# Kernel tuning notes

Hardware: AMD Instinct MI355X
Metric: run time of the kernel (lower is better)

Reference implementation:

```python
import jax, jax.numpy as jnp
import numpy as np

IN_C, DIM, OUT_C, N_PIECES = 3, 256, 256, 20
BATCH, SET_N = 16, 128


def _xavier(k, shape, fan_in, fan_out):
    limit = float(np.sqrt(6.0 / (fan_in + fan_out)))
    return jax.random.uniform(k, shape, jnp.float32, -limit, limit)


def setup_inputs() -> dict:
    key = jax.random.key(0)
    ks = jax.random.split(key, 9)
    return {
        "x": jax.random.normal(ks[0], (BATCH, IN_C, SET_N), jnp.float32),
        "conv1_w": _xavier(ks[1], (DIM, IN_C), IN_C, DIM),
        "conv1_b": jnp.zeros((DIM,), jnp.float32),
        "conv2_w": _xavier(ks[2], (DIM, DIM), DIM, DIM),
        "conv2_b": jnp.zeros((DIM,), jnp.float32),
        "pool_w": jax.random.normal(ks[3], (DIM, N_PIECES + 1), jnp.float32) * 0.1,
        "lin1_w": _xavier(ks[4], (DIM, DIM), DIM, DIM),
        "lin1_b": jnp.zeros((DIM,), jnp.float32),
        "lin2_w": _xavier(ks[5], (OUT_C, DIM), DIM, OUT_C),
        "lin2_b": jnp.zeros((OUT_C,), jnp.float32),
        "cls1_w": _xavier(ks[6], (OUT_C, OUT_C), OUT_C, OUT_C),
        "cls1_b": jnp.zeros((OUT_C,), jnp.float32),
        "cls2_w": _xavier(ks[7], (10, OUT_C), OUT_C, 10),
        "cls2_b": jnp.zeros((10,), jnp.float32),
    }


def _fspool(x, pool_w, tau=1.0):
    # x: (B, C, N); pool_w: (C, N_PIECES+1). n is None -> full sets, mask is all ones.
    B, C, N = x.shape
    # piecewise-linear continuous weights evaluated at ratios i/(N-1)
    ratios = jnp.clip(jnp.arange(N, dtype=x.dtype) / max(N - 1, 1), 0.0, 1.0)  # (N,)
    idx_f = N_PIECES * ratios
    idx = jnp.floor(idx_f).astype(jnp.int32)
    frac = idx_f - idx.astype(x.dtype)
    left = pool_w[:, idx]                                   # (C, N)
    right = pool_w[:, jnp.clip(idx + 1, 0, N_PIECES)]       # (C, N)
    w = (1.0 - frac) * left + frac * right                  # (C, N)
    # relaxed continuous sort (NeuralSort / deterministic_sort), descending
    s = x.reshape(B * C, N, 1)
    A = jnp.abs(s - jnp.swapaxes(s, 1, 2))                  # (BC, N, N)
    Bsum = A.sum(axis=2, keepdims=True)                     # == A @ 1 1^T rowsums, (BC, N, 1)
    scaling = (N + 1 - 2 * (jnp.arange(N) + 1)).astype(x.dtype)  # (N,)
    Cmat = s * scaling[None, None, :]                       # (BC, N, N)
    P = jax.nn.softmax(jnp.swapaxes(Cmat - Bsum, 1, 2) / tau, axis=-1)  # (BC, N, N)
    xs = jnp.matmul(P, s).reshape(B, C, N)                  # soft-sorted, descending
    pooled = (xs * w[None]).sum(axis=2)                     # (B, C)
    return pooled, P


def reference(x, conv1_w, conv1_b, conv2_w, conv2_b, pool_w,
              lin1_w, lin1_b, lin2_w, lin2_b, cls1_w, cls1_b, cls2_w, cls2_b):
    # conv1x1 stack: (B, IN_C, N) -> (B, DIM, N)
    h = jnp.einsum('dc,bcn->bdn', conv1_w, x) + conv1_b[None, :, None]
    h = jax.nn.relu(h)
    h = jnp.einsum('dc,bcn->bdn', conv2_w, h) + conv2_b[None, :, None]
    pooled, _ = _fspool(h, pool_w)                          # (B, DIM)
    z = jax.nn.relu(pooled @ lin1_w.T + lin1_b)
    z = z @ lin2_w.T + lin2_b                               # (B, OUT_C)
    z = jax.nn.relu(z @ cls1_w.T + cls1_b)
    return z @ cls2_w.T + cls2_b                            # (B, 10)
```

## Files before the change

### kernel.cpp

```cpp
#include <hip/hip_runtime.h>
#include <math.h>


#if __has_builtin(__builtin_amdgcn_exp2f)
#define EXP2F(x) __builtin_amdgcn_exp2f(x)
#else
#define EXP2F(x) exp2f(x)
#endif

__device__ __forceinline__ float pool_weight(const float* __restrict__ pw, int j)
{
    float ratio = (float)j / 127.0f;
    float idx_f = 20.0f * ratio;
    int idx = (int)idx_f;
    float frac = idx_f - (float)idx;
    int idx2 = idx + 1 > 20 ? 20 : idx + 1;
    return (1.0f - frac) * pw[idx] + frac * pw[idx2];
}

#define OSTEP(sv, bv, scal, m, se, sd)                      \
    {                                                       \
        float v_  = fmaf((sv), (scal), -(bv));              \
        float mn_ = fmaxf((m), v_);                         \
        float sc_ = EXP2F((m) - mn_);                       \
        float e_  = EXP2F(v_ - mn_);                        \
        (se) = fmaf((se), sc_, e_);                         \
        (sd) = fmaf((sd), sc_, e_ * (sv));                  \
        (m)  = mn_;                                         \
    }

__global__ __launch_bounds__(256) void conv_pool_kernel(
    const float* __restrict__ x,   const float* __restrict__ w1,
    const float* __restrict__ b1,  const float* __restrict__ W2,
    const float* __restrict__ b2,  const float* __restrict__ pool_w,
    float* __restrict__ pooled)
{
    const float LOG2E = 1.4426950408889634f;
    __shared__ float4 w1p[256];
    __shared__ float  Ast[4][32];
    __shared__ float2 Bsp[32][66];
    __shared__ float  ss[4][128];
    __shared__ float  bb[4][128];

    int tid = threadIdx.x;
    int blk = blockIdx.x;
    int b   = blk >> 6;
    int c0  = (blk & 63) << 2;

    int wid = tid >> 6, l = tid & 63;
    int ng  = tid & 31;
    int kg  = tid >> 5;
    int n0  = ng * 2;

    w1p[tid] = make_float4(w1[tid*3], w1[tid*3+1], w1[tid*3+2], b1[tid]);
    const float* xb = x + b * 384;
    float x00 = xb[n0],          x01 = xb[n0 + 1];
    float x0a = xb[n0 + 64],     x0b = xb[n0 + 65];
    float x10 = xb[128 + n0],    x11 = xb[128 + n0 + 1];
    float x1a = xb[128 + n0 + 64], x1b = xb[128 + n0 + 65];
    float x20 = xb[256 + n0],    x21 = xb[256 + n0 + 1];
    float x2a = xb[256 + n0 + 64], x2b = xb[256 + n0 + 65];
    __syncthreads();

    float acc0 = 0.f, acc1 = 0.f;

    for (int k0 = 0; k0 < 256; k0 += 32) {
        if (tid < 128)
            Ast[tid >> 5][tid & 31] =
                W2[(c0 + (tid >> 5)) * 256 + k0 + (tid & 31)];
        #pragma unroll
        for (int q = 0; q < 4; q++) {
            int krel = kg * 4 + q;
            float4 wv = w1p[k0 + krel];
            float h0 = fmaxf(fmaf(wv.x,x00, fmaf(wv.y,x10, fmaf(wv.z,x20, wv.w))), 0.f);
            float h1 = fmaxf(fmaf(wv.x,x01, fmaf(wv.y,x11, fmaf(wv.z,x21, wv.w))), 0.f);
            float ha = fmaxf(fmaf(wv.x,x0a, fmaf(wv.y,x1a, fmaf(wv.z,x2a, wv.w))), 0.f);
            float hb = fmaxf(fmaf(wv.x,x0b, fmaf(wv.y,x1b, fmaf(wv.z,x2b, wv.w))), 0.f);
            *(float4*)&Bsp[krel][n0] = make_float4(h0, ha, h1, hb);
        }
        __syncthreads();
        float4 a4[8];
        #pragma unroll
        for (int q = 0; q < 8; q++)
            a4[q] = *(const float4*)&Ast[wid][q * 4];
        #pragma unroll
        for (int kk = 0; kk < 32; kk++) {
            float a = ((const float*)a4)[kk];
            float2 bv = Bsp[kk][l];
            acc0 = fmaf(a, bv.x, acc0);
            acc1 = fmaf(a, bv.y, acc1);
        }
        __syncthreads();
    }

    float bias = b2[c0 + wid];
    float s0 = acc0 + bias, s1 = acc1 + bias;
    ss[wid][l]      = s0;
    ss[wid][l + 64] = s1;

    float a0=0,a1=0,a2=0,a3=0, g0=0,g1=0,g2=0,g3=0;
    #pragma unroll 8
    for (int j = 0; j < 128; j += 4) {
        float4 s4 = *(const float4*)&ss[wid][j];
        a0 += fabsf(s0 - s4.x); a1 += fabsf(s0 - s4.y);
        a2 += fabsf(s0 - s4.z); a3 += fabsf(s0 - s4.w);
        g0 += fabsf(s1 - s4.x); g1 += fabsf(s1 - s4.y);
        g2 += fabsf(s1 - s4.z); g3 += fabsf(s1 - s4.w);
    }
    bb[wid][l]      = ((a0+a1)+(a2+a3)) * LOG2E;
    bb[wid][l + 64] = ((g0+g1)+(g2+g3)) * LOG2E;

    float scal0 = (float)(127 - 2 * l) * LOG2E;
    float scal1 = (float)(-1 - 2 * l) * LOG2E;
    float mA0=-1e30f, mB0=-1e30f, mA1=-1e30f, mB1=-1e30f;
    float seA0=0,seB0=0,sdA0=0,sdB0=0;
    float seA1=0,seB1=0,sdA1=0,sdB1=0;
    #pragma unroll 4
    for (int i = 0; i < 128; i += 4) {
        float4 s4 = *(const float4*)&ss[wid][i];
        float4 b4 = *(const float4*)&bb[wid][i];
        OSTEP(s4.x, b4.x, scal0, mA0, seA0, sdA0);
        OSTEP(s4.y, b4.y, scal0, mB0, seB0, sdB0);
        OSTEP(s4.z, b4.z, scal0, mA0, seA0, sdA0);
        OSTEP(s4.w, b4.w, scal0, mB0, seB0, sdB0);
        OSTEP(s4.x, b4.x, scal1, mA1, seA1, sdA1);
        OSTEP(s4.y, b4.y, scal1, mB1, seB1, sdB1);
        OSTEP(s4.z, b4.z, scal1, mA1, seA1, sdA1);
        OSTEP(s4.w, b4.w, scal1, mB1, seB1, sdB1);
    }
    float m0  = fmaxf(mA0, mB0);
    float scA = EXP2F(mA0 - m0), scB = EXP2F(mB0 - m0);
    float xs0 = (sdA0 * scA + sdB0 * scB) / (seA0 * scA + seB0 * scB);
    float m1  = fmaxf(mA1, mB1);
    float tA  = EXP2F(mA1 - m1), tB = EXP2F(mB1 - m1);
    float xs1 = (sdA1 * tA + sdB1 * tB) / (seA1 * tA + seB1 * tB);

    int c = c0 + wid;
    const float* pw = pool_w + c * 21;
    float part = xs0 * pool_weight(pw, l) + xs1 * pool_weight(pw, l + 64);
    #pragma unroll
    for (int off = 32; off > 0; off >>= 1)
        part += __shfl_xor(part, off);
    if (l == 0) pooled[b * 256 + c] = part;
}

__device__ __forceinline__ void dense512(
    const float* __restrict__ W, const float* __restrict__ Bv,
    const float* in_lds, float* out_lds, int tid, bool do_relu)
{
    int o = tid >> 1, p = tid & 1;
    const float* wr = W + o * 256 + p * 128;
    const float* ir = in_lds + p * 128;
    float acc = 0.f;
    #pragma unroll
    for (int k = 0; k < 128; k += 4) {
        float4 wv = *(const float4*)(wr + k);
        float4 iv = *(const float4*)(ir + k);
        acc = fmaf(wv.x, iv.x, acc); acc = fmaf(wv.y, iv.y, acc);
        acc = fmaf(wv.z, iv.z, acc); acc = fmaf(wv.w, iv.w, acc);
    }
    acc += __shfl_xor(acc, 1);
    if (p == 0) {
        acc += Bv[o];
        out_lds[o] = do_relu ? fmaxf(acc, 0.f) : acc;
    }
}

__global__ __launch_bounds__(512) void tail_kernel(
    const float* __restrict__ pooled,
    const float* __restrict__ L1w, const float* __restrict__ L1b,
    const float* __restrict__ L2w, const float* __restrict__ L2b,
    const float* __restrict__ C1w, const float* __restrict__ C1b,
    const float* __restrict__ C2w, const float* __restrict__ C2b,
    float* __restrict__ out)
{
    __shared__ float za[256], zb[256];
    int bt = blockIdx.x, tid = threadIdx.x;
    if (tid < 256) za[tid] = pooled[bt * 256 + tid];
    __syncthreads();
    dense512(L1w, L1b, za, zb, tid, true);
    __syncthreads();
    dense512(L2w, L2b, zb, za, tid, false);
    __syncthreads();
    dense512(C1w, C1b, za, zb, tid, true);
    __syncthreads();
    if (tid < 320) {
        int o = tid >> 5, kb = tid & 31;
        const float* wr = C2w + o * 256 + kb * 8;
        const float* ir = zb + kb * 8;
        float4 w0 = *(const float4*)(wr);
        float4 w1v = *(const float4*)(wr + 4);
        float4 i0 = *(const float4*)(ir);
        float4 i1 = *(const float4*)(ir + 4);
        float p = fmaf(w0.x,i0.x, fmaf(w0.y,i0.y, fmaf(w0.z,i0.z,
                  fmaf(w0.w,i0.w, fmaf(w1v.x,i1.x, fmaf(w1v.y,i1.y,
                  fmaf(w1v.z,i1.z, w1v.w*i1.w)))))));
        #pragma unroll
        for (int off = 16; off > 0; off >>= 1)
            p += __shfl_xor(p, off, 32);
        if (kb == 0) out[bt * 10 + o] = p + C2b[o];
    }
}

extern "C" void kernel_launch(void* const* d_in, const int* in_sizes, int n_in,
                              void* d_out, int out_size, void* d_ws, size_t ws_size,
                              hipStream_t stream)
{
    (void)in_sizes; (void)n_in; (void)out_size; (void)ws_size;
    const float* x       = (const float*)d_in[0];
    const float* conv1_w = (const float*)d_in[1];
    const float* conv1_b = (const float*)d_in[2];
    const float* conv2_w = (const float*)d_in[3];
    const float* conv2_b = (const float*)d_in[4];
    const float* pool_w  = (const float*)d_in[5];
    const float* lin1_w  = (const float*)d_in[6];
    const float* lin1_b  = (const float*)d_in[7];
    const float* lin2_w  = (const float*)d_in[8];
    const float* lin2_b  = (const float*)d_in[9];
    const float* cls1_w  = (const float*)d_in[10];
    const float* cls1_b  = (const float*)d_in[11];
    const float* cls2_w  = (const float*)d_in[12];
    const float* cls2_b  = (const float*)d_in[13];
    float* out = (float*)d_out;

    float* pooled = (float*)d_ws;

    conv_pool_kernel<<<1024, 256, 0, stream>>>(
        x, conv1_w, conv1_b, conv2_w, conv2_b, pool_w, pooled);
    tail_kernel<<<16, 512, 0, stream>>>(pooled,
        lin1_w, lin1_b, lin2_w, lin2_b, cls1_w, cls1_b, cls2_w, cls2_b, out);
}
```

Measured before the change: 62.61 us.

## Fuse MLP tail into conv-pool kernel via last-blocks atomic counter gate

Merges the two kernels into one launch. Each block publishes its pooled value and increments a global counter, and the last 16 blocks to arrive each wait for all blocks to finish before running the dense MLP tail for one batch element. This removes the second kernel launch and its gap, but adds a memset launch, a spin-wait, and a serial 256-thread tail running inside the final blocks.

New measurement: 70.12 us. 1.12x slower.

```diff
diff --git a/kernel.cpp b/kernel.cpp
--- a/kernel.cpp
+++ b/kernel.cpp
@@ -7,6 +7,8 @@
 #else
 #define EXP2F(x) exp2f(x)
 #endif
+
+#define NBLK 1024u
 
 __device__ __forceinline__ float pool_weight(const float* __restrict__ pw, int j)
 {
@@ -29,11 +31,16 @@
         (m)  = mn_;                                         \
     }
 
-__global__ __launch_bounds__(256) void conv_pool_kernel(
+__global__ __launch_bounds__(256) void fused_lastgate(
     const float* __restrict__ x,   const float* __restrict__ w1,
     const float* __restrict__ b1,  const float* __restrict__ W2,
     const float* __restrict__ b2,  const float* __restrict__ pool_w,
-    float* __restrict__ pooled)
+    const float* __restrict__ L1w, const float* __restrict__ L1b,
+    const float* __restrict__ L2w, const float* __restrict__ L2b,
+    const float* __restrict__ C1w, const float* __restrict__ C1b,
+    const float* __restrict__ C2w, const float* __restrict__ C2b,
+    float* __restrict__ pooled, unsigned* __restrict__ cnt,
+    float* __restrict__ out)
 {
     const float LOG2E = 1.4426950408889634f;
     __shared__ float4 w1p[256];
@@ -41,6 +48,8 @@
     __shared__ float2 Bsp[32][66];
     __shared__ float  ss[4][128];
     __shared__ float  bb[4][128];
+    __shared__ float  za[256], zb[256];
+    __shared__ unsigned sOld;
 
     int tid = threadIdx.x;
     int blk = blockIdx.x;
@@ -54,11 +63,11 @@
 
     w1p[tid] = make_float4(w1[tid*3], w1[tid*3+1], w1[tid*3+2], b1[tid]);
     const float* xb = x + b * 384;
-    float x00 = xb[n0],          x01 = xb[n0 + 1];
-    float x0a = xb[n0 + 64],     x0b = xb[n0 + 65];
-    float x10 = xb[128 + n0],    x11 = xb[128 + n0 + 1];
+    float x00 = xb[n0],            x01 = xb[n0 + 1];
+    float x0a = xb[n0 + 64],       x0b = xb[n0 + 65];
+    float x10 = xb[128 + n0],      x11 = xb[128 + n0 + 1];
     float x1a = xb[128 + n0 + 64], x1b = xb[128 + n0 + 65];
-    float x20 = xb[256 + n0],    x21 = xb[256 + n0 + 1];
+    float x20 = xb[256 + n0],      x21 = xb[256 + n0 + 1];
     float x2a = xb[256 + n0 + 64], x2b = xb[256 + n0 + 65];
     __syncthreads();
 
@@ -141,64 +150,80 @@
     #pragma unroll
     for (int off = 32; off > 0; off >>= 1)
         part += __shfl_xor(part, off);
-    if (l == 0) pooled[b * 256 + c] = part;
-}
-
-__device__ __forceinline__ void dense512(
-    const float* __restrict__ W, const float* __restrict__ Bv,
-    const float* in_lds, float* out_lds, int tid, bool do_relu)
-{
-    int o = tid >> 1, p = tid & 1;
-    const float* wr = W + o * 256 + p * 128;
-    const float* ir = in_lds + p * 128;
-    float acc = 0.f;
-    #pragma unroll
-    for (int k = 0; k < 128; k += 4) {
-        float4 wv = *(const float4*)(wr + k);
-        float4 iv = *(const float4*)(ir + k);
-        acc = fmaf(wv.x, iv.x, acc); acc = fmaf(wv.y, iv.y, acc);
-        acc = fmaf(wv.z, iv.z, acc); acc = fmaf(wv.w, iv.w, acc);
-    }
-    acc += __shfl_xor(acc, 1);
-    if (p == 0) {
-        acc += Bv[o];
-        out_lds[o] = do_relu ? fmaxf(acc, 0.f) : acc;
-    }
-}
-
-__global__ __launch_bounds__(512) void tail_kernel(
-    const float* __restrict__ pooled,
-    const float* __restrict__ L1w, const float* __restrict__ L1b,
-    const float* __restrict__ L2w, const float* __restrict__ L2b,
-    const float* __restrict__ C1w, const float* __restrict__ C1b,
-    const float* __restrict__ C2w, const float* __restrict__ C2b,
-    float* __restrict__ out)
-{
-    __shared__ float za[256], zb[256];
-    int bt = blockIdx.x, tid = threadIdx.x;
-    if (tid < 256) za[tid] = pooled[bt * 256 + tid];
-    __syncthreads();
-    dense512(L1w, L1b, za, zb, tid, true);
-    __syncthreads();
-    dense512(L2w, L2b, zb, za, tid, false);
-    __syncthreads();
-    dense512(C1w, C1b, za, zb, tid, true);
-    __syncthreads();
-    if (tid < 320) {
-        int o = tid >> 5, kb = tid & 31;
-        const float* wr = C2w + o * 256 + kb * 8;
-        const float* ir = zb + kb * 8;
-        float4 w0 = *(const float4*)(wr);
-        float4 w1v = *(const float4*)(wr + 4);
-        float4 i0 = *(const float4*)(ir);
-        float4 i1 = *(const float4*)(ir + 4);
-        float p = fmaf(w0.x,i0.x, fmaf(w0.y,i0.y, fmaf(w0.z,i0.z,
-                  fmaf(w0.w,i0.w, fmaf(w1v.x,i1.x, fmaf(w1v.y,i1.y,
-                  fmaf(w1v.z,i1.z, w1v.w*i1.w)))))));
-        #pragma unroll
-        for (int off = 16; off > 0; off >>= 1)
-            p += __shfl_xor(p, off, 32);
-        if (kb == 0) out[bt * 10 + o] = p + C2b[o];
+    if (l == 0)
+        __hip_atomic_store(&pooled[b * 256 + c], part,
+                           __ATOMIC_RELAXED, __HIP_MEMORY_SCOPE_AGENT);
+
+    __syncthreads();
+    if (tid == 0)
+        sOld = __hip_atomic_fetch_add(cnt, 1u, __ATOMIC_ACQ_REL,
+                                      __HIP_MEMORY_SCOPE_AGENT);
+    __syncthreads();
+    unsigned old = sOld;
+    if (old < NBLK - 16u) return;
+
+    int bt = (int)(old - (NBLK - 16u));
+    if (tid == 0 && old != NBLK - 1u) {
+        while (__hip_atomic_load(cnt, __ATOMIC_ACQUIRE,
+                                 __HIP_MEMORY_SCOPE_AGENT) < NBLK)
+            __builtin_amdgcn_s_sleep(2);
+    }
+    __syncthreads();
+
+    za[tid] = __hip_atomic_load(&pooled[bt * 256 + tid],
+                                __ATOMIC_RELAXED, __HIP_MEMORY_SCOPE_AGENT);
+    __syncthreads();
+    {
+        float acc = L1b[tid];
+        const float* wr = L1w + tid * 256;
+        #pragma unroll 8
+        for (int k = 0; k < 256; k += 4) {
+            float4 wv = *(const float4*)(wr + k);
+            float4 iv = *(const float4*)(&za[k]);
+            acc = fmaf(wv.x, iv.x, acc); acc = fmaf(wv.y, iv.y, acc);
+            acc = fmaf(wv.z, iv.z, acc); acc = fmaf(wv.w, iv.w, acc);
+        }
+        zb[tid] = fmaxf(acc, 0.f);
+    }
+    __syncthreads();
+    {
+        float acc = L2b[tid];
+        const float* wr = L2w + tid * 256;
+        #pragma unroll 8
+        for (int k = 0; k < 256; k += 4) {
+            float4 wv = *(const float4*)(wr + k);
+            float4 iv = *(const float4*)(&zb[k]);
+            acc = fmaf(wv.x, iv.x, acc); acc = fmaf(wv.y, iv.y, acc);
+            acc = fmaf(wv.z, iv.z, acc); acc = fmaf(wv.w, iv.w, acc);
+        }
+        za[tid] = acc;
+    }
+    __syncthreads();
+    {
+        float acc = C1b[tid];
+        const float* wr = C1w + tid * 256;
+        #pragma unroll 8
+        for (int k = 0; k < 256; k += 4) {
+            float4 wv = *(const float4*)(wr + k);
+            float4 iv = *(const float4*)(&za[k]);
+            acc = fmaf(wv.x, iv.x, acc); acc = fmaf(wv.y, iv.y, acc);
+            acc = fmaf(wv.z, iv.z, acc); acc = fmaf(wv.w, iv.w, acc);
+        }
+        zb[tid] = fmaxf(acc, 0.f);
+    }
+    __syncthreads();
+    if (tid < 160) {
+        int o = tid >> 4, kk = tid & 15;
+        const float* wr = C2w + o * 256;
+        float pp = 0.f;
+        #pragma unroll
+        for (int k = kk * 16; k < kk * 16 + 16; k++)
+            pp = fmaf(zb[k], wr[k], pp);
+        pp += __shfl_down(pp, 8, 16);
+        pp += __shfl_down(pp, 4, 16);
+        pp += __shfl_down(pp, 2, 16);
+        pp += __shfl_down(pp, 1, 16);
+        if (kk == 0) out[bt * 10 + o] = pp + C2b[o];
     }
 }
 
@@ -223,10 +248,12 @@
     const float* cls2_b  = (const float*)d_in[13];
     float* out = (float*)d_out;
 
-    float* pooled = (float*)d_ws;
-
-    conv_pool_kernel<<<1024, 256, 0, stream>>>(
-        x, conv1_w, conv1_b, conv2_w, conv2_b, pool_w, pooled);
-    tail_kernel<<<16, 512, 0, stream>>>(pooled,
-        lin1_w, lin1_b, lin2_w, lin2_b, cls1_w, cls1_b, cls2_w, cls2_b, out);
+    float*    pooled = (float*)d_ws;
+    unsigned* cnt    = (unsigned*)((float*)d_ws + 4096);
+
+    hipMemsetAsync(cnt, 0, sizeof(unsigned), stream);
+    fused_lastgate<<<NBLK, 256, 0, stream>>>(
+        x, conv1_w, conv1_b, conv2_w, conv2_b, pool_w,
+        lin1_w, lin1_b, lin2_w, lin2_b, cls1_w, cls1_b, cls2_w, cls2_b,
+        pooled, cnt, out);
 }
```

## Use two-pass softmax and halve channels per block in conv-pool kernel

Applied to the files above, without the earlier changes.

Each block now handles 2 channels instead of 4, so the grid doubles to 2048 blocks, and the four waves split the 128 sort rows of the two channels. The online softmax with per-step rescaling (two exp2 per element) becomes a max pass followed by an exp/sum pass (one exp2 per element), and the two halves are combined through shared memory. Only two of four waves do the conv2 GEMM, and each block recomputes the conv1 activations for its batch, so that redundant conv1 work doubles. Launch bounds now request 8 blocks per CU.

After: 65.57 us. +4.7%, slower.

```diff
diff --git a/kernel.cpp b/kernel.cpp
--- a/kernel.cpp
+++ b/kernel.cpp
@@ -18,59 +18,49 @@
     return (1.0f - frac) * pw[idx] + frac * pw[idx2];
 }
 
-#define OSTEP(sv, bv, scal, m, se, sd)                      \
-    {                                                       \
-        float v_  = fmaf((sv), (scal), -(bv));              \
-        float mn_ = fmaxf((m), v_);                         \
-        float sc_ = EXP2F((m) - mn_);                       \
-        float e_  = EXP2F(v_ - mn_);                        \
-        (se) = fmaf((se), sc_, e_);                         \
-        (sd) = fmaf((sd), sc_, e_ * (sv));                  \
-        (m)  = mn_;                                         \
-    }
-
-__global__ __launch_bounds__(256) void conv_pool_kernel(
+__global__ __launch_bounds__(256, 8) void conv_pool_kernel(
     const float* __restrict__ x,   const float* __restrict__ w1,
     const float* __restrict__ b1,  const float* __restrict__ W2,
     const float* __restrict__ b2,  const float* __restrict__ pool_w,
     float* __restrict__ pooled)
 {
     const float LOG2E = 1.4426950408889634f;
-    __shared__ float4 w1p[256];
-    __shared__ float  Ast[4][32];
-    __shared__ float2 Bsp[32][66];
-    __shared__ float  ss[4][128];
-    __shared__ float  bb[4][128];
+    __shared__ __align__(16) float4 w1p[256];
+    __shared__ __align__(16) float  Ast[2][16];
+    __shared__ __align__(16) float2 Bsp[16][66];
+    __shared__ __align__(16) float  ss[2][128];
+    __shared__ __align__(16) float  bb[2][128];
+    __shared__ float partial[4];
 
     int tid = threadIdx.x;
     int blk = blockIdx.x;
-    int b   = blk >> 6;
-    int c0  = (blk & 63) << 2;
+    int b   = blk >> 7;
+    int c0  = (blk & 127) << 1;
 
     int wid = tid >> 6, l = tid & 63;
-    int ng  = tid & 31;
-    int kg  = tid >> 5;
+    int r   = wid & 1,  h = wid >> 1;
+    int ng  = tid & 31, kg = tid >> 5;
     int n0  = ng * 2;
 
     w1p[tid] = make_float4(w1[tid*3], w1[tid*3+1], w1[tid*3+2], b1[tid]);
     const float* xb = x + b * 384;
-    float x00 = xb[n0],          x01 = xb[n0 + 1];
-    float x0a = xb[n0 + 64],     x0b = xb[n0 + 65];
-    float x10 = xb[128 + n0],    x11 = xb[128 + n0 + 1];
+    float x00 = xb[n0],            x01 = xb[n0 + 1];
+    float x0a = xb[n0 + 64],       x0b = xb[n0 + 65];
+    float x10 = xb[128 + n0],      x11 = xb[128 + n0 + 1];
     float x1a = xb[128 + n0 + 64], x1b = xb[128 + n0 + 65];
-    float x20 = xb[256 + n0],    x21 = xb[256 + n0 + 1];
+    float x20 = xb[256 + n0],      x21 = xb[256 + n0 + 1];
     float x2a = xb[256 + n0 + 64], x2b = xb[256 + n0 + 65];
     __syncthreads();
 
     float acc0 = 0.f, acc1 = 0.f;
 
-    for (int k0 = 0; k0 < 256; k0 += 32) {
-        if (tid < 128)
-            Ast[tid >> 5][tid & 31] =
-                W2[(c0 + (tid >> 5)) * 256 + k0 + (tid & 31)];
+    for (int k0 = 0; k0 < 256; k0 += 16) {
+        if (tid < 32)
+            Ast[tid >> 4][tid & 15] =
+                W2[(c0 + (tid >> 4)) * 256 + k0 + (tid & 15)];
         #pragma unroll
-        for (int q = 0; q < 4; q++) {
-            int krel = kg * 4 + q;
+        for (int q = 0; q < 2; q++) {
+            int krel = kg * 2 + q;
             float4 wv = w1p[k0 + krel];
             float h0 = fmaxf(fmaf(wv.x,x00, fmaf(wv.y,x10, fmaf(wv.z,x20, wv.w))), 0.f);
             float h1 = fmaxf(fmaf(wv.x,x01, fmaf(wv.y,x11, fmaf(wv.z,x21, wv.w))), 0.f);
@@ -79,69 +69,80 @@
             *(float4*)&Bsp[krel][n0] = make_float4(h0, ha, h1, hb);
         }
         __syncthreads();
-        float4 a4[8];
-        #pragma unroll
-        for (int q = 0; q < 8; q++)
-            a4[q] = *(const float4*)&Ast[wid][q * 4];
-        #pragma unroll
-        for (int kk = 0; kk < 32; kk++) {
-            float a = ((const float*)a4)[kk];
-            float2 bv = Bsp[kk][l];
-            acc0 = fmaf(a, bv.x, acc0);
-            acc1 = fmaf(a, bv.y, acc1);
+        if (wid < 2) {
+            float4 a4[4];
+            #pragma unroll
+            for (int q = 0; q < 4; q++)
+                a4[q] = *(const float4*)&Ast[wid][q * 4];
+            #pragma unroll
+            for (int kk = 0; kk < 16; kk++) {
+                float a = ((const float*)a4)[kk];
+                float2 bv = Bsp[kk][l];
+                acc0 = fmaf(a, bv.x, acc0);
+                acc1 = fmaf(a, bv.y, acc1);
+            }
         }
         __syncthreads();
     }
 
-    float bias = b2[c0 + wid];
-    float s0 = acc0 + bias, s1 = acc1 + bias;
-    ss[wid][l]      = s0;
-    ss[wid][l + 64] = s1;
-
-    float a0=0,a1=0,a2=0,a3=0, g0=0,g1=0,g2=0,g3=0;
+    if (wid < 2) {
+        float bias = b2[c0 + wid];
+        ss[wid][l]      = acc0 + bias;
+        ss[wid][l + 64] = acc1 + bias;
+    }
+    __syncthreads();
+
+    int i = h * 64 + l;
+    float si = ss[r][i];
+
+    float a0 = 0.f, a1 = 0.f, a2 = 0.f, a3 = 0.f;
     #pragma unroll 8
     for (int j = 0; j < 128; j += 4) {
-        float4 s4 = *(const float4*)&ss[wid][j];
-        a0 += fabsf(s0 - s4.x); a1 += fabsf(s0 - s4.y);
-        a2 += fabsf(s0 - s4.z); a3 += fabsf(s0 - s4.w);
-        g0 += fabsf(s1 - s4.x); g1 += fabsf(s1 - s4.y);
-        g2 += fabsf(s1 - s4.z); g3 += fabsf(s1 - s4.w);
-    }
-    bb[wid][l]      = ((a0+a1)+(a2+a3)) * LOG2E;
-    bb[wid][l + 64] = ((g0+g1)+(g2+g3)) * LOG2E;
-
-    float scal0 = (float)(127 - 2 * l) * LOG2E;
-    float scal1 = (float)(-1 - 2 * l) * LOG2E;
-    float mA0=-1e30f, mB0=-1e30f, mA1=-1e30f, mB1=-1e30f;
-    float seA0=0,seB0=0,sdA0=0,sdB0=0;
-    float seA1=0,seB1=0,sdA1=0,sdB1=0;
+        float4 s4 = *(const float4*)&ss[r][j];
+        a0 += fabsf(si - s4.x); a1 += fabsf(si - s4.y);
+        a2 += fabsf(si - s4.z); a3 += fabsf(si - s4.w);
+    }
+    bb[r][i] = ((a0 + a1) + (a2 + a3)) * LOG2E;
+    __syncthreads();
+
+    float scal = (float)(127 - 2 * i) * LOG2E;
+    float m0 = -1e30f, m1 = -1e30f, m2 = -1e30f, m3 = -1e30f;
+    #pragma unroll 8
+    for (int k = 0; k < 128; k += 4) {
+        float4 s4 = *(const float4*)&ss[r][k];
+        float4 b4 = *(const float4*)&bb[r][k];
+        m0 = fmaxf(m0, fmaf(s4.x, scal, -b4.x));
+        m1 = fmaxf(m1, fmaf(s4.y, scal, -b4.y));
+        m2 = fmaxf(m2, fmaf(s4.z, scal, -b4.z));
+        m3 = fmaxf(m3, fmaf(s4.w, scal, -b4.w));
+    }
+    float m = fmaxf(fmaxf(m0, m1), fmaxf(m2, m3));
+
+    float se0 = 0.f, se1 = 0.f, se2 = 0.f, se3 = 0.f;
+    float sd0 = 0.f, sd1 = 0.f, sd2 = 0.f, sd3 = 0.f;
     #pragma unroll 4
-    for (int i = 0; i < 128; i += 4) {
-        float4 s4 = *(const float4*)&ss[wid][i];
-        float4 b4 = *(const float4*)&bb[wid][i];
-        OSTEP(s4.x, b4.x, scal0, mA0, seA0, sdA0);
-        OSTEP(s4.y, b4.y, scal0, mB0, seB0, sdB0);
-        OSTEP(s4.z, b4.z, scal0, mA0, seA0, sdA0);
-        OSTEP(s4.w, b4.w, scal0, mB0, seB0, sdB0);
-        OSTEP(s4.x, b4.x, scal1, mA1, seA1, sdA1);
-        OSTEP(s4.y, b4.y, scal1, mB1, seB1, sdB1);
-        OSTEP(s4.z, b4.z, scal1, mA1, seA1, sdA1);
-        OSTEP(s4.w, b4.w, scal1, mB1, seB1, sdB1);
-    }
-    float m0  = fmaxf(mA0, mB0);
-    float scA = EXP2F(mA0 - m0), scB = EXP2F(mB0 - m0);
-    float xs0 = (sdA0 * scA + sdB0 * scB) / (seA0 * scA + seB0 * scB);
-    float m1  = fmaxf(mA1, mB1);
-    float tA  = EXP2F(mA1 - m1), tB = EXP2F(mB1 - m1);
-    float xs1 = (sdA1 * tA + sdB1 * tB) / (seA1 * tA + seB1 * tB);
-
-    int c = c0 + wid;
-    const float* pw = pool_w + c * 21;
-    float part = xs0 * pool_weight(pw, l) + xs1 * pool_weight(pw, l + 64);
+    for (int k = 0; k < 128; k += 4) {
+        float4 s4 = *(const float4*)&ss[r][k];
+        float4 b4 = *(const float4*)&bb[r][k];
+        float e0 = EXP2F(fmaf(s4.x, scal, -b4.x) - m);
+        float e1 = EXP2F(fmaf(s4.y, scal, -b4.y) - m);
+        float e2 = EXP2F(fmaf(s4.z, scal, -b4.z) - m);
+        float e3 = EXP2F(fmaf(s4.w, scal, -b4.w) - m);
+        se0 += e0; sd0 = fmaf(e0, s4.x, sd0);
+        se1 += e1; sd1 = fmaf(e1, s4.y, sd1);
+        se2 += e2; sd2 = fmaf(e2, s4.z, sd2);
+        se3 += e3; sd3 = fmaf(e3, s4.w, sd3);
+    }
+    float xs = ((sd0 + sd1) + (sd2 + sd3)) / ((se0 + se1) + (se2 + se3));
+
+    float part = xs * pool_weight(pool_w + (c0 + r) * 21, i);
     #pragma unroll
     for (int off = 32; off > 0; off >>= 1)
         part += __shfl_xor(part, off);
-    if (l == 0) pooled[b * 256 + c] = part;
+    if (l == 0) partial[wid] = part;
+    __syncthreads();
+    if (tid < 2)
+        pooled[b * 256 + c0 + tid] = partial[tid] + partial[tid + 2];
 }
 
 __device__ __forceinline__ void dense512(
@@ -225,7 +226,7 @@
 
     float* pooled = (float*)d_ws;
 
-    conv_pool_kernel<<<1024, 256, 0, stream>>>(
+    conv_pool_kernel<<<2048, 256, 0, stream>>>(
         x, conv1_w, conv1_b, conv2_w, conv2_b, pool_w, pooled);
     tail_kernel<<<16, 512, 0, stream>>>(pooled,
         lin1_w, lin1_b, lin2_w, lin2_b, cls1_w, cls1_b, cls2_w, cls2_b, out);
```
